# Kernel tuning notes

Measured on AMD Instinct MI355X. Metric: run time of the kernel, lower is better.

Reference implementation:

```python
import jax, jax.numpy as jnp
import numpy as np

B, T, N, H = 4, 256, 16, 256
NHEAD = 8
FFN = 1024
WIN = 8
EPS = 1e-5


def setup_inputs() -> dict:
    key = jax.random.key(0)
    ks = jax.random.split(key, 10)
    s = 0.02
    return {
        "x": jax.random.normal(ks[0], (B, T, N, H), dtype=jnp.float32),
        "key_padding_mask": jnp.zeros((B, T, N), dtype=bool),
        "Wq": jax.random.normal(ks[1], (H, H), dtype=jnp.float32) * s,
        "bq": jnp.zeros((H,), dtype=jnp.float32),
        "Wk": jax.random.normal(ks[2], (H, H), dtype=jnp.float32) * s,
        "bk": jnp.zeros((H,), dtype=jnp.float32),
        "Wv": jax.random.normal(ks[3], (H, H), dtype=jnp.float32) * s,
        "bv": jnp.zeros((H,), dtype=jnp.float32),
        "W1": jax.random.normal(ks[4], (H, FFN), dtype=jnp.float32) * s,
        "b1": jnp.zeros((FFN,), dtype=jnp.float32),
        "W2": jax.random.normal(ks[5], (FFN, H), dtype=jnp.float32) * s,
        "b2": jnp.zeros((H,), dtype=jnp.float32),
        "g1": jnp.ones((H,), dtype=jnp.float32),
        "beta1": jnp.zeros((H,), dtype=jnp.float32),
        "g2": jnp.ones((H,), dtype=jnp.float32),
        "beta2": jnp.zeros((H,), dtype=jnp.float32),
    }


def _layer_norm(x, g, b):
    m = jnp.mean(x, axis=-1, keepdims=True)
    v = jnp.mean(jnp.square(x - m), axis=-1, keepdims=True)
    return (x - m) * jax.lax.rsqrt(v + EPS) * g + b


def reference(x, key_padding_mask, Wq, bq, Wk, bk, Wv, bv, W1, b1, W2, b2, g1, beta1, g2, beta2):
    Bq, Tq, Nq, Hq = x.shape
    D = Hq // NHEAD
    W = 2 * WIN + 1
    # projections
    q = (x @ Wq + bq).reshape(Bq, Tq, Nq, NHEAD, D) / np.float32(np.sqrt(D))
    k = (x @ Wk + bk).reshape(Bq, Tq, Nq, NHEAD, D)
    v = (x @ Wv + bv).reshape(Bq, Tq, Nq, NHEAD, D)
    idx = jnp.arange(Tq)[:, None] + jnp.arange(W)[None, :] - WIN  # (T, W)
    valid = (idx >= 0) & (idx < Tq)                               # (T, W)
    cidx = jnp.clip(idx, 0, Tq - 1)
    vf6 = valid.reshape(1, Tq, W, 1, 1, 1).astype(q.dtype)
    # gathered window keys/values, zero outside clip: (B, T, W, N, h, D)
    wk = jnp.take(k, cidx, axis=1) * vf6
    wv = jnp.take(v, cidx, axis=1) * vf6
    # attention logits over (W, N) neighbors per head
    logits = jnp.einsum('btnhd,btwmhd->btnwmh', q, wk)  # (B,T,N,W,N,h)
    # mask: padded detections within window, plus out-of-range frames
    kpm_g = jnp.take(key_padding_mask, cidx, axis=1)          # (B,T,W,N)
    mask = jnp.where(valid[None, :, :, None], kpm_g, True)    # (B,T,W,N)
    logits = jnp.where(mask[:, :, None, :, :, None], -jnp.inf, logits)
    attn = jax.nn.softmax(logits.reshape(Bq, Tq, Nq, W * Nq, NHEAD), axis=-2)
    ctx = jnp.einsum('btnmh,btmhd->btnhd', attn,
                     wv.reshape(Bq, Tq, W * Nq, NHEAD, D)).reshape(Bq, Tq, Nq, Hq)
    # residual + LN + FFN + residual + LN (dropout = identity in eval)
    y = _layer_norm(x + ctx, g1, beta1)
    ff = jax.nn.relu(y @ W1 + b1) @ W2 + b2
    return _layer_norm(y + ff, g2, beta2)
```

## Files before the change

kernel.cpp:

```cpp
#include <hip/hip_runtime.h>
#include <hip/hip_bf16.h>
#include <math.h>

typedef __attribute__((ext_vector_type(8))) short short8;
typedef __attribute__((ext_vector_type(4))) float float4v;

#define BB 4
#define TT 256
#define NDET 16
#define HH 256
#define NHEAD 8
#define DD 32
#define FFNDIM 1024
#define ROWS (BB*TT*NDET)
#define EPS 1e-5f

__device__ __forceinline__ unsigned short f2bf(float f) {
  unsigned int u = __float_as_uint(f);
  u += 0x7fffu + ((u >> 16) & 1u);
  return (unsigned short)(u >> 16);
}
__device__ __forceinline__ float bf2f(unsigned short u) {
  return __uint_as_float((unsigned int)u << 16);
}
__device__ __forceinline__ float exp2v(float x) {
  float r; asm("v_exp_f32 %0, %1" : "=v"(r) : "v"(x)); return r;
}
__device__ __forceinline__ unsigned int cvtpk(float lo, float hi) {
  unsigned int r; asm("v_cvt_pk_bf16_f32 %0, %1, %2" : "=v"(r) : "v"(lo), "v"(hi)); return r;
}

__device__ __forceinline__ void wt_tile(const float* __restrict__ W, unsigned short* __restrict__ WT,
                                        int K, int N, int k0, int n0,
                                        float (*tile)[33], int tid) {
  {
    int r = tid >> 3, c4 = (tid & 7) * 4;
    float4 in = *(const float4*)(W + (size_t)(k0 + r) * N + n0 + c4);
    tile[r][c4 + 0] = in.x; tile[r][c4 + 1] = in.y;
    tile[r][c4 + 2] = in.z; tile[r][c4 + 3] = in.w;
  }
  __syncthreads();
  {
    int n = tid >> 3, k4 = (tid & 7) * 4;
    ushort4 o;
    o.x = f2bf(tile[k4 + 0][n]); o.y = f2bf(tile[k4 + 1][n]);
    o.z = f2bf(tile[k4 + 2][n]); o.w = f2bf(tile[k4 + 3][n]);
    *(ushort4*)(WT + (size_t)(n0 + n) * K + k0 + k4) = o;
  }
}

__global__ void prep_kernel(const float* __restrict__ x, const unsigned char* __restrict__ kpm,
                            const float* __restrict__ Wq, const float* __restrict__ Wk,
                            const float* __restrict__ Wv, const float* __restrict__ W1,
                            const float* __restrict__ W2,
                            const float* __restrict__ bq, const float* __restrict__ bk,
                            const float* __restrict__ bv,
                            unsigned short* __restrict__ xb, unsigned short* __restrict__ WqkvT,
                            unsigned short* __restrict__ W1T, unsigned short* __restrict__ W2T,
                            unsigned short* __restrict__ kpm16, float* __restrict__ bqkv) {
  __shared__ float tile[32][33];
  int bid = blockIdx.x, tid = threadIdx.x;
  if (bid < 2048) {
    size_t i = (size_t)(bid * 256 + tid) * 8;
    float4 v0 = *(const float4*)(x + i);
    float4 v1 = *(const float4*)(x + i + 4);
    ushort4 o0 = { f2bf(v0.x), f2bf(v0.y), f2bf(v0.z), f2bf(v0.w) };
    ushort4 o1 = { f2bf(v1.x), f2bf(v1.y), f2bf(v1.z), f2bf(v1.w) };
    *(ushort4*)(xb + i) = o0;
    *(ushort4*)(xb + i + 4) = o1;
  } else if (bid < 2240) {
    int t = bid - 2048;
    int wsel = t >> 6, tt = t & 63;
    const float* W = (wsel == 0) ? Wq : (wsel == 1) ? Wk : Wv;
    wt_tile(W, WqkvT + wsel * 65536, 256, 256, (tt >> 3) * 32, (tt & 7) * 32, tile, tid);
  } else if (bid < 2496) {
    int tt = bid - 2240;
    wt_tile(W1, W1T, 256, 1024, (tt >> 5) * 32, (tt & 31) * 32, tile, tid);
  } else if (bid < 2752) {
    int tt = bid - 2496;
    wt_tile(W2, W2T, 1024, 256, (tt >> 3) * 32, (tt & 7) * 32, tile, tid);
  } else if (bid < 2756) {
    int w = (bid - 2752) * 256 + tid;
    uint4 u = *(const uint4*)(kpm + (size_t)w * 16);
    unsigned int a[4] = {u.x, u.y, u.z, u.w};
    unsigned int bits = 0;
#pragma unroll
    for (int m = 0; m < 16; ++m)
      if ((a[m >> 2] >> ((m & 3) * 8)) & 0xffu) bits |= (1u << m);
    kpm16[w] = (unsigned short)bits;
  } else {
    bqkv[tid] = bq[tid];
    bqkv[256 + tid] = bk[tid];
    bqkv[512 + tid] = bv[tid];
  }
}

template<int NROWS, int K, int NT>
__device__ __forceinline__ void stage_rows(const unsigned short* __restrict__ src, int kcol0,
                                           char* ldsbase, int tid) {
  constexpr int ISS = NROWS * 8 / NT;
  int wave = tid >> 6;
#pragma unroll
  for (int i = 0; i < ISS; ++i) {
    int flat = i * (NT * 16) + tid * 16;
    int r = flat >> 7;
    int cb = flat & 127;
    int scb = cb ^ ((r & 7) << 4);
    const unsigned short* g = src + (size_t)r * K + kcol0 + (scb >> 1);
    char* l = ldsbase + i * (NT * 16) + wave * 1024;
    __builtin_amdgcn_global_load_lds((const __attribute__((address_space(1))) void*)g,
                                     (__attribute__((address_space(3))) void*)l, 16, 0, 0);
  }
}

template<int EPI>
__launch_bounds__(256, 4)
__global__ void gemm_kernel(const unsigned short* __restrict__ A,
                            const unsigned short* __restrict__ Bt,
                            const float* __restrict__ bias,
                            unsigned short* __restrict__ q_o, unsigned short* __restrict__ k_o,
                            unsigned short* __restrict__ vT_o,
                            unsigned short* __restrict__ outb) {
  constexpr int BM = 128, BN = 128, K = 256, KP = K / 64;
  __shared__ char smem[(BM + BN) * 128];
  const int tid = threadIdx.x;
  const int wave = tid >> 6, lane = tid & 63;
  const int lrow = lane & 15, g = lane >> 4;
  const int m0 = blockIdx.x * BM;
  const int n0 = blockIdx.y * BN;
  const int wr = wave >> 1, wc = wave & 1;
  char* As = smem;
  char* Bs = smem + BM * 128;
  float4v acc[4][4];
#pragma unroll
  for (int i = 0; i < 4; ++i)
#pragma unroll
    for (int j = 0; j < 4; ++j) acc[i][j] = (float4v){0.f, 0.f, 0.f, 0.f};

  const unsigned short* Abase = A + (size_t)m0 * K;
  const unsigned short* Bbase = Bt + (size_t)n0 * K;
  for (int ph = 0; ph < KP; ++ph) {
    if (ph) __syncthreads();
    stage_rows<BM, K, 256>(Abase, ph * 64, As, tid);
    stage_rows<BN, K, 256>(Bbase, ph * 64, Bs, tid);
    __syncthreads();
#pragma unroll
    for (int ks = 0; ks < 2; ++ks) {
      short8 af[4], bf[4];
#pragma unroll
      for (int i = 0; i < 4; ++i) {
        int ar = wr * 64 + i * 16 + lrow;
        af[i] = *(const short8*)(As + ar * 128 + ((ks * 64 + g * 16) ^ ((ar & 7) << 4)));
      }
#pragma unroll
      for (int j = 0; j < 4; ++j) {
        int br = wc * 64 + j * 16 + lrow;
        bf[j] = *(const short8*)(Bs + br * 128 + ((ks * 64 + g * 16) ^ ((br & 7) << 4)));
      }
#pragma unroll
      for (int i = 0; i < 4; ++i)
#pragma unroll
        for (int j = 0; j < 4; ++j)
          acc[i][j] = __builtin_amdgcn_mfma_f32_16x16x32_bf16(af[i], bf[j], acc[i][j], 0, 0, 0);
    }
  }

  if (EPI == 0) {
    const float QS = 0.17677669529663687f * 1.4426950408889634f;
#pragma unroll
    for (int i = 0; i < 4; ++i)
#pragma unroll
      for (int j = 0; j < 4; ++j) {
        int C = n0 + wc * 64 + j * 16 + lrow;
        float bv = bias[C];
        int proj = C >> 8, cc = C & 255;
        int h = cc >> 5, d = cc & 31;
        if (proj == 2) {
          int grow0 = m0 + wr * 64 + i * 16 + g * 4;
          int b = grow0 >> 12, tn0 = grow0 & 4095;
          ushort4 o;
          o.x = f2bf(acc[i][j][0] + bv);
          o.y = f2bf(acc[i][j][1] + bv);
          o.z = f2bf(acc[i][j][2] + bv);
          o.w = f2bf(acc[i][j][3] + bv);
          *(ushort4*)(vT_o + ((size_t)(b * 8 + h) * 32 + d) * 4096 + tn0) = o;
        } else {
          unsigned short* om = (proj == 0) ? q_o : k_o;
          float sc = (proj == 0) ? QS : 1.f;
#pragma unroll
          for (int r = 0; r < 4; ++r) {
            int grow = m0 + wr * 64 + i * 16 + g * 4 + r;
            int b = grow >> 12, tn = grow & 4095;
            om[(size_t)((b * 8 + h) * 4096 + tn) * 32 + d] = f2bf((acc[i][j][r] + bv) * sc);
          }
        }
      }
  } else {
#pragma unroll
    for (int i = 0; i < 4; ++i)
#pragma unroll
      for (int j = 0; j < 4; ++j) {
        int C = n0 + wc * 64 + j * 16 + lrow;
        float bv = bias[C];
#pragma unroll
        for (int r = 0; r < 4; ++r) {
          int grow = m0 + wr * 64 + i * 16 + g * 4 + r;
          outb[(size_t)grow * FFNDIM + C] = f2bf(fmaxf(acc[i][j][r] + bv, 0.f));
        }
      }
  }
}

__launch_bounds__(512, 4)
__global__ void attn_ln_kernel(const unsigned short* __restrict__ qb,
                               const unsigned short* __restrict__ kb,
                               const unsigned short* __restrict__ vT,
                               const unsigned short* __restrict__ kpm16,
                               const unsigned short* __restrict__ xb,
                               const float* __restrict__ gw, const float* __restrict__ bw,
                               unsigned short* __restrict__ yb) {
  __shared__ char Pall[8][9216];
  __shared__ float stats[8][16][2];
  __shared__ float mst[16], rst[16];
  int tid = threadIdx.x;
  int wave = tid >> 6, l = tid & 63;
  int lid = (blockIdx.x & 7) * 128 + (blockIdx.x >> 3);
  int t = lid & 255, b = lid >> 8;
  char* P = Pall[wave];
  int lrow = l & 15, g = l >> 4;
  int swz = (lrow & 3) << 4;
  size_t base = (size_t)(b * 8 + wave) * 4096;
  short8 qf = *(const short8*)(qb + (base + t * 16 + lrow) * 32 + g * 8);
  const float4v z4 = {0.f, 0.f, 0.f, 0.f};
  float4v s[17];
  float mx = -INFINITY;
#pragma unroll
  for (int w = 0; w < 17; ++w) {
    int j = t + w - 8;
    if (j >= 0 && j < 256) {
      short8 kf = *(const short8*)(kb + (base + j * 16 + lrow) * 32 + g * 8);
      float4v sv = __builtin_amdgcn_mfma_f32_16x16x32_bf16(kf, qf, z4, 0, 0, 0);
      unsigned int mw = kpm16[b * 256 + j];
#pragma unroll
      for (int r = 0; r < 4; ++r)
        if ((mw >> (g * 4 + r)) & 1u) sv[r] = -INFINITY;
      s[w] = sv;
#pragma unroll
      for (int r = 0; r < 4; ++r) mx = fmaxf(mx, sv[r]);
    } else {
      s[w] = (float4v){-INFINITY, -INFINITY, -INFINITY, -INFINITY};
    }
  }
  mx = fmaxf(mx, __shfl_xor(mx, 16));
  mx = fmaxf(mx, __shfl_xor(mx, 32));
  float sum = 0.f;
#pragma unroll
  for (int w = 0; w < 17; ++w)
#pragma unroll
    for (int r = 0; r < 4; ++r) {
      float e = exp2v(s[w][r] - mx);
      s[w][r] = e; sum += e;
    }
  sum += __shfl_xor(sum, 16);
  sum += __shfl_xor(sum, 32);
  float inv = 1.f / sum;
#pragma unroll
  for (int w = 0; w < 17; ++w) {
    unsigned int u0 = cvtpk(s[w][0], s[w][1]);
    unsigned int u1 = cvtpk(s[w][2], s[w][3]);
    *(unsigned int*)(P + lrow * 576 + (((w * 16 + g * 4 + 0) * 2) ^ swz)) = u0;
    *(unsigned int*)(P + lrow * 576 + (((w * 16 + g * 4 + 2) * 2) ^ swz)) = u1;
  }
  *(unsigned int*)(P + lrow * 576 + (((272 + g * 4 + 0) * 2) ^ swz)) = 0u;
  *(unsigned int*)(P + lrow * 576 + (((272 + g * 4 + 2) * 2) ^ swz)) = 0u;

  size_t rowbase = (size_t)(b * 256 + t) * 16 * 256;
  int col = wave * 32 + lrow;
  float xv0[4], xv1[4];
#pragma unroll
  for (int r = 0; r < 4; ++r) {
    xv0[r] = bf2f(xb[rowbase + (g * 4 + r) * 256 + col]);
    xv1[r] = bf2f(xb[rowbase + (g * 4 + r) * 256 + col + 16]);
  }

  asm volatile("s_waitcnt lgkmcnt(0)" ::: "memory");
  __builtin_amdgcn_sched_barrier(0);
  float4v o0 = z4, o1 = z4;
  int tn0 = (t - 8) * 16;
  const unsigned short* vbase = vT + (base * 32 / 4096 + lrow) * 4096;
  __builtin_amdgcn_s_setprio(1);
#pragma unroll
  for (int c = 0; c < 9; ++c) {
    short8 pf = *(const short8*)(P + lrow * 576 + ((c * 64 + g * 16) ^ swz));
    short8 v0 = *(const short8*)(vbase + tn0 + c * 32 + g * 8);
    short8 v1 = *(const short8*)(vbase + (size_t)16 * 4096 + tn0 + c * 32 + g * 8);
    o0 = __builtin_amdgcn_mfma_f32_16x16x32_bf16(pf, v0, o0, 0, 0, 0);
    o1 = __builtin_amdgcn_mfma_f32_16x16x32_bf16(pf, v1, o1, 0, 0, 0);
  }
  __builtin_amdgcn_s_setprio(0);

  float va0[4], va1[4];
#pragma unroll
  for (int r = 0; r < 4; ++r) {
    float invn = __shfl(inv, g * 4 + r);
    va0[r] = o0[r] * invn + xv0[r];
    va1[r] = o1[r] * invn + xv1[r];
  }
#pragma unroll
  for (int r = 0; r < 4; ++r) {
    float sm = va0[r] + va1[r];
    float sq = va0[r] * va0[r] + va1[r] * va1[r];
#pragma unroll
    for (int off = 1; off < 16; off <<= 1) {
      sm += __shfl_xor(sm, off);
      sq += __shfl_xor(sq, off);
    }
    if (lrow == 0) {
      stats[wave][g * 4 + r][0] = sm;
      stats[wave][g * 4 + r][1] = sq;
    }
  }
  __syncthreads();
  if (tid < 16) {
    float S = 0.f, Q = 0.f;
#pragma unroll
    for (int w2 = 0; w2 < 8; ++w2) { S += stats[w2][tid][0]; Q += stats[w2][tid][1]; }
    float mean = S * (1.f / 256.f);
    float var = Q * (1.f / 256.f) - mean * mean;
    mst[tid] = mean;
    rst[tid] = rsqrtf(var + EPS);
  }
  __syncthreads();
  float gv0 = gw[col], gv1 = gw[col + 16];
  float bv0 = bw[col], bv1 = bw[col + 16];
#pragma unroll
  for (int r = 0; r < 4; ++r) {
    int row = g * 4 + r;
    float mean = mst[row], rs = rst[row];
    yb[rowbase + row * 256 + col]      = f2bf((va0[r] - mean) * rs * gv0 + bv0);
    yb[rowbase + row * 256 + col + 16] = f2bf((va1[r] - mean) * rs * gv1 + bv1);
  }
}

__launch_bounds__(512, 4)
__global__ void ffn2_kernel(const unsigned short* __restrict__ hid,
                            const unsigned short* __restrict__ W2T,
                            const float* __restrict__ b2,
                            const unsigned short* __restrict__ yb,
                            const float* __restrict__ gw, const float* __restrict__ bw,
                            float* __restrict__ out) {
  constexpr int BM = 32, BN = 256, K = 1024, KP = K / 64;
  __shared__ char smem[(BM + BN) * 128];
  __shared__ float stats[8][16][2];
  __shared__ float mst[32], rst[32];
  const int tid = threadIdx.x;
  const int wave = tid >> 6, lane = tid & 63;
  const int lrow = lane & 15, g = lane >> 4;
  const int m0 = blockIdx.x * BM;
  const int wr = wave >> 2, wc = wave & 3;
  char* As = smem;
  char* Bs = smem + BM * 128;
  float4v acc[4];
#pragma unroll
  for (int j = 0; j < 4; ++j) acc[j] = (float4v){0.f, 0.f, 0.f, 0.f};

  const unsigned short* Abase = hid + (size_t)m0 * K;
  for (int ph = 0; ph < KP; ++ph) {
    if (ph) __syncthreads();
    if (tid < 256) {
      int flat = tid * 16;
      int r = flat >> 7;
      int cb = flat & 127;
      int scb = cb ^ ((r & 7) << 4);
      const unsigned short* gp = Abase + (size_t)r * K + ph * 64 + (scb >> 1);
      char* lp = As + wave * 1024;
      __builtin_amdgcn_global_load_lds((const __attribute__((address_space(1))) void*)gp,
                                       (__attribute__((address_space(3))) void*)lp, 16, 0, 0);
    }
    stage_rows<BN, K, 512>(W2T, ph * 64, Bs, tid);
    __syncthreads();
#pragma unroll
    for (int ks = 0; ks < 2; ++ks) {
      short8 af, bf[4];
      {
        int ar = wr * 16 + lrow;
        af = *(const short8*)(As + ar * 128 + ((ks * 64 + g * 16) ^ ((ar & 7) << 4)));
      }
#pragma unroll
      for (int j = 0; j < 4; ++j) {
        int br = wc * 64 + j * 16 + lrow;
        bf[j] = *(const short8*)(Bs + br * 128 + ((ks * 64 + g * 16) ^ ((br & 7) << 4)));
      }
#pragma unroll
      for (int j = 0; j < 4; ++j)
        acc[j] = __builtin_amdgcn_mfma_f32_16x16x32_bf16(af, bf[j], acc[j], 0, 0, 0);
    }
  }
  __syncthreads();

#pragma unroll
  for (int j = 0; j < 4; ++j) {
    int col = wc * 64 + j * 16 + lrow;
    float bv = b2[col];
#pragma unroll
    for (int r = 0; r < 4; ++r) {
      int row = wr * 16 + g * 4 + r;
      acc[j][r] += bv + bf2f(yb[(size_t)(m0 + row) * 256 + col]);
    }
  }
#pragma unroll
  for (int r = 0; r < 4; ++r) {
    float sm = acc[0][r] + acc[1][r] + acc[2][r] + acc[3][r];
    float sq = acc[0][r] * acc[0][r] + acc[1][r] * acc[1][r]
             + acc[2][r] * acc[2][r] + acc[3][r] * acc[3][r];
#pragma unroll
    for (int off = 1; off < 16; off <<= 1) {
      sm += __shfl_xor(sm, off);
      sq += __shfl_xor(sq, off);
    }
    if (lrow == 0) {
      stats[wave][g * 4 + r][0] = sm;
      stats[wave][g * 4 + r][1] = sq;
    }
  }
  __syncthreads();
  if (tid < 32) {
    int wrr = tid >> 4;
    float S = 0.f, Q = 0.f;
#pragma unroll
    for (int w2 = 0; w2 < 4; ++w2) {
      S += stats[wrr * 4 + w2][tid & 15][0];
      Q += stats[wrr * 4 + w2][tid & 15][1];
    }
    float mean = S * (1.f / 256.f);
    float var = Q * (1.f / 256.f) - mean * mean;
    mst[tid] = mean;
    rst[tid] = rsqrtf(var + EPS);
  }
  __syncthreads();
#pragma unroll
  for (int r = 0; r < 4; ++r) {
    int rl = wr * 16 + g * 4 + r;
    float mean = mst[rl], rs = rst[rl];
#pragma unroll
    for (int j = 0; j < 4; ++j) {
      int col = wc * 64 + j * 16 + lrow;
      out[(size_t)(m0 + rl) * 256 + col] = (acc[j][r] - mean) * rs * gw[col] + bw[col];
    }
  }
}

extern "C" void kernel_launch(void* const* d_in, const int* in_sizes, int n_in,
                              void* d_out, int out_size, void* d_ws, size_t ws_size,
                              hipStream_t stream) {
  const float* x  = (const float*)d_in[0];
  const unsigned char* kpm = (const unsigned char*)d_in[1];
  const float* Wq = (const float*)d_in[2];
  const float* bq = (const float*)d_in[3];
  const float* Wk = (const float*)d_in[4];
  const float* bk = (const float*)d_in[5];
  const float* Wv = (const float*)d_in[6];
  const float* bv = (const float*)d_in[7];
  const float* W1 = (const float*)d_in[8];
  const float* b1 = (const float*)d_in[9];
  const float* W2 = (const float*)d_in[10];
  const float* b2 = (const float*)d_in[11];
  const float* g1 = (const float*)d_in[12];
  const float* be1= (const float*)d_in[13];
  const float* g2 = (const float*)d_in[14];
  const float* be2= (const float*)d_in[15];
  float* out = (float*)d_out;

  char* w = (char*)d_ws;
  const size_t MB = 1u << 20;
  unsigned short* xb   = (unsigned short*)(w);
  unsigned short* qhm  = (unsigned short*)(w + 8 * MB);
  unsigned short* khm  = (unsigned short*)(w + 16 * MB);
  unsigned short* vTb  = (unsigned short*)(w + 24 * MB);
  unsigned short* yb   = (unsigned short*)(w + 48 * MB);
  unsigned short* WqkvT = (unsigned short*)(w + 72 * MB);
  unsigned short* W1T = WqkvT + 196608;
  unsigned short* W2T = W1T + 262144;
  unsigned short* kpm16 = W2T + 262144;
  float* bqkv = (float*)(kpm16 + 1024);
  unsigned short* hid = qhm;

  prep_kernel<<<2757, 256, 0, stream>>>(x, kpm, Wq, Wk, Wv, W1, W2, bq, bk, bv,
                                        xb, WqkvT, W1T, W2T, kpm16, bqkv);
  gemm_kernel<0><<<dim3(128, 6), 256, 0, stream>>>(xb, WqkvT, bqkv, qhm, khm, vTb, nullptr);
  attn_ln_kernel<<<1024, 512, 0, stream>>>(qhm, khm, vTb, kpm16, xb, g1, be1, yb);
  gemm_kernel<1><<<dim3(128, 8), 256, 0, stream>>>(yb, W1T, b1, nullptr, nullptr, nullptr, hid);
  ffn2_kernel<<<512, 512, 0, stream>>>(hid, W2T, b2, yb, g2, be2, out);
}
```

Before: 101.0 us.

## Split windowed attention into two online-softmax halves to cut registers and LDS

The 17-frame attention window is now processed in two passes (8 frames, then 9), with online-softmax rescaling of the partial output and sum between them. This shrinks the score register array from 17 to 9 float4 and the per-wave LDS probability buffer from 9216 to 5120 bytes, aiming for higher occupancy or less register pressure. In exchange it adds a rescale step, an extra LDS wait and serialization between the halves, and explicit -inf to zero handling.

```diff
diff --git a/kernel.cpp b/kernel.cpp
--- a/kernel.cpp
+++ b/kernel.cpp
@@ -219,7 +219,7 @@
                                const unsigned short* __restrict__ xb,
                                const float* __restrict__ gw, const float* __restrict__ bw,
                                unsigned short* __restrict__ yb) {
-  __shared__ char Pall[8][9216];
+  __shared__ char Pall[8][5120];
   __shared__ float stats[8][16][2];
   __shared__ float mst[16], rst[16];
   int tid = threadIdx.x;
@@ -232,12 +232,15 @@
   size_t base = (size_t)(b * 8 + wave) * 4096;
   short8 qf = *(const short8*)(qb + (base + t * 16 + lrow) * 32 + g * 8);
   const float4v z4 = {0.f, 0.f, 0.f, 0.f};
-  float4v s[17];
-  float mx = -INFINITY;
-#pragma unroll
-  for (int w = 0; w < 17; ++w) {
+  int tn0 = (t - 8) * 16;
+  const unsigned short* vbase = vT + ((size_t)(b * 8 + wave) * 32 + lrow) * 4096;
+
+  float4v s[9];
+  float mx1 = -INFINITY;
+#pragma unroll
+  for (int w = 0; w < 8; ++w) {
     int j = t + w - 8;
-    if (j >= 0 && j < 256) {
+    if (j >= 0) {
       short8 kf = *(const short8*)(kb + (base + j * 16 + lrow) * 32 + g * 8);
       float4v sv = __builtin_amdgcn_mfma_f32_16x16x32_bf16(kf, qf, z4, 0, 0, 0);
       unsigned int mw = kpm16[b * 256 + j];
@@ -246,59 +249,113 @@
         if ((mw >> (g * 4 + r)) & 1u) sv[r] = -INFINITY;
       s[w] = sv;
 #pragma unroll
-      for (int r = 0; r < 4; ++r) mx = fmaxf(mx, sv[r]);
+      for (int r = 0; r < 4; ++r) mx1 = fmaxf(mx1, sv[r]);
     } else {
       s[w] = (float4v){-INFINITY, -INFINITY, -INFINITY, -INFINITY};
     }
   }
-  mx = fmaxf(mx, __shfl_xor(mx, 16));
-  mx = fmaxf(mx, __shfl_xor(mx, 32));
+  mx1 = fmaxf(mx1, __shfl_xor(mx1, 16));
+  mx1 = fmaxf(mx1, __shfl_xor(mx1, 32));
   float sum = 0.f;
 #pragma unroll
-  for (int w = 0; w < 17; ++w)
+  for (int w = 0; w < 8; ++w)
 #pragma unroll
     for (int r = 0; r < 4; ++r) {
-      float e = exp2v(s[w][r] - mx);
+      float e = exp2v(s[w][r] - mx1);
+      e = (s[w][r] == -INFINITY) ? 0.f : e;
       s[w][r] = e; sum += e;
     }
-  sum += __shfl_xor(sum, 16);
-  sum += __shfl_xor(sum, 32);
-  float inv = 1.f / sum;
-#pragma unroll
-  for (int w = 0; w < 17; ++w) {
+#pragma unroll
+  for (int w = 0; w < 8; ++w) {
     unsigned int u0 = cvtpk(s[w][0], s[w][1]);
     unsigned int u1 = cvtpk(s[w][2], s[w][3]);
-    *(unsigned int*)(P + lrow * 576 + (((w * 16 + g * 4 + 0) * 2) ^ swz)) = u0;
-    *(unsigned int*)(P + lrow * 576 + (((w * 16 + g * 4 + 2) * 2) ^ swz)) = u1;
-  }
-  *(unsigned int*)(P + lrow * 576 + (((272 + g * 4 + 0) * 2) ^ swz)) = 0u;
-  *(unsigned int*)(P + lrow * 576 + (((272 + g * 4 + 2) * 2) ^ swz)) = 0u;
-
-  size_t rowbase = (size_t)(b * 256 + t) * 16 * 256;
-  int col = wave * 32 + lrow;
-  float xv0[4], xv1[4];
-#pragma unroll
-  for (int r = 0; r < 4; ++r) {
-    xv0[r] = bf2f(xb[rowbase + (g * 4 + r) * 256 + col]);
-    xv1[r] = bf2f(xb[rowbase + (g * 4 + r) * 256 + col + 16]);
-  }
-
+    *(unsigned int*)(P + lrow * 320 + (((w * 16 + g * 4 + 0) * 2) ^ swz)) = u0;
+    *(unsigned int*)(P + lrow * 320 + (((w * 16 + g * 4 + 2) * 2) ^ swz)) = u1;
+  }
   asm volatile("s_waitcnt lgkmcnt(0)" ::: "memory");
   __builtin_amdgcn_sched_barrier(0);
   float4v o0 = z4, o1 = z4;
-  int tn0 = (t - 8) * 16;
-  const unsigned short* vbase = vT + (base * 32 / 4096 + lrow) * 4096;
   __builtin_amdgcn_s_setprio(1);
 #pragma unroll
-  for (int c = 0; c < 9; ++c) {
-    short8 pf = *(const short8*)(P + lrow * 576 + ((c * 64 + g * 16) ^ swz));
+  for (int c = 0; c < 4; ++c) {
+    short8 pf = *(const short8*)(P + lrow * 320 + ((c * 64 + g * 16) ^ swz));
     short8 v0 = *(const short8*)(vbase + tn0 + c * 32 + g * 8);
     short8 v1 = *(const short8*)(vbase + (size_t)16 * 4096 + tn0 + c * 32 + g * 8);
     o0 = __builtin_amdgcn_mfma_f32_16x16x32_bf16(pf, v0, o0, 0, 0, 0);
     o1 = __builtin_amdgcn_mfma_f32_16x16x32_bf16(pf, v1, o1, 0, 0, 0);
   }
   __builtin_amdgcn_s_setprio(0);
-
+  asm volatile("s_waitcnt lgkmcnt(0)" ::: "memory");
+  __builtin_amdgcn_sched_barrier(0);
+
+  float mx2 = -INFINITY;
+  float4v s2[9];
+#pragma unroll
+  for (int w = 0; w < 9; ++w) {
+    int j = t + w;
+    if (j < 256) {
+      short8 kf = *(const short8*)(kb + (base + j * 16 + lrow) * 32 + g * 8);
+      float4v sv = __builtin_amdgcn_mfma_f32_16x16x32_bf16(kf, qf, z4, 0, 0, 0);
+      unsigned int mw = kpm16[b * 256 + j];
+#pragma unroll
+      for (int r = 0; r < 4; ++r)
+        if ((mw >> (g * 4 + r)) & 1u) sv[r] = -INFINITY;
+      s2[w] = sv;
+#pragma unroll
+      for (int r = 0; r < 4; ++r) mx2 = fmaxf(mx2, sv[r]);
+    } else {
+      s2[w] = (float4v){-INFINITY, -INFINITY, -INFINITY, -INFINITY};
+    }
+  }
+  mx2 = fmaxf(mx2, __shfl_xor(mx2, 16));
+  mx2 = fmaxf(mx2, __shfl_xor(mx2, 32));
+  float mxT = fmaxf(mx1, mx2);
+  float sc1 = (mx1 == -INFINITY) ? 0.f : exp2v(mx1 - mxT);
+  sum *= sc1;
+#pragma unroll
+  for (int r = 0; r < 4; ++r) { o0[r] *= sc1; o1[r] *= sc1; }
+#pragma unroll
+  for (int w = 0; w < 9; ++w)
+#pragma unroll
+    for (int r = 0; r < 4; ++r) {
+      float e = (s2[w][r] == -INFINITY) ? 0.f : exp2v(s2[w][r] - mxT);
+      s2[w][r] = e; sum += e;
+    }
+#pragma unroll
+  for (int w = 0; w < 9; ++w) {
+    unsigned int u0 = cvtpk(s2[w][0], s2[w][1]);
+    unsigned int u1 = cvtpk(s2[w][2], s2[w][3]);
+    *(unsigned int*)(P + lrow * 320 + (((w * 16 + g * 4 + 0) * 2) ^ swz)) = u0;
+    *(unsigned int*)(P + lrow * 320 + (((w * 16 + g * 4 + 2) * 2) ^ swz)) = u1;
+  }
+  *(unsigned int*)(P + lrow * 320 + (((144 + g * 4 + 0) * 2) ^ swz)) = 0u;
+  *(unsigned int*)(P + lrow * 320 + (((144 + g * 4 + 2) * 2) ^ swz)) = 0u;
+
+  size_t rowbase = (size_t)(b * 256 + t) * 16 * 256;
+  int col = wave * 32 + lrow;
+  float xv0[4], xv1[4];
+#pragma unroll
+  for (int r = 0; r < 4; ++r) {
+    xv0[r] = bf2f(xb[rowbase + (g * 4 + r) * 256 + col]);
+    xv1[r] = bf2f(xb[rowbase + (g * 4 + r) * 256 + col + 16]);
+  }
+
+  asm volatile("s_waitcnt lgkmcnt(0)" ::: "memory");
+  __builtin_amdgcn_sched_barrier(0);
+  __builtin_amdgcn_s_setprio(1);
+#pragma unroll
+  for (int c = 0; c < 5; ++c) {
+    short8 pf = *(const short8*)(P + lrow * 320 + ((c * 64 + g * 16) ^ swz));
+    short8 v0 = *(const short8*)(vbase + tn0 + 128 + c * 32 + g * 8);
+    short8 v1 = *(const short8*)(vbase + (size_t)16 * 4096 + tn0 + 128 + c * 32 + g * 8);
+    o0 = __builtin_amdgcn_mfma_f32_16x16x32_bf16(pf, v0, o0, 0, 0, 0);
+    o1 = __builtin_amdgcn_mfma_f32_16x16x32_bf16(pf, v1, o1, 0, 0, 0);
+  }
+  __builtin_amdgcn_s_setprio(0);
+
+  sum += __shfl_xor(sum, 16);
+  sum += __shfl_xor(sum, 32);
+  float inv = 1.f / sum;
   float va0[4], va1[4];
 #pragma unroll
   for (int r = 0; r < 4; ++r) {
```

Result: slower. 109.6 us (+8.5%).
